# Performance work log

Measured on AMD Instinct MI355X. Metric: run time of the kernel, lower is better.

The kernel has to match this reference:

```python
import jax, jax.numpy as jnp
import numpy as np

NEG_SLOPE = 0.2  # PyG GATConv LeakyReLU slope
HEADS = 4

def _gat_conv(x, edge_index, W, a_src, a_dst, b):
    """Single-relation GATConv (PyG semantics, concat=True).
    x: [N, Fin]; edge_index: [2, E]; W: [Fin, H*D]; a_src/a_dst: [H, D]; b: [H*D].
    """
    N = x.shape[0]
    H, D = a_src.shape
    h = (x @ W).reshape(N, H, D)                      # [N, H, D]
    src, dst = edge_index[0], edge_index[1]
    # per-node attention halves
    al_s = jnp.einsum('nhd,hd->nh', h, a_src)         # [N, H]
    al_d = jnp.einsum('nhd,hd->nh', h, a_dst)         # [N, H]
    alpha = jax.nn.leaky_relu(al_s[src] + al_d[dst], NEG_SLOPE)  # [E, H]
    # segment softmax over incoming edges per destination node
    amax = jax.ops.segment_max(alpha, dst, num_segments=N)       # [N, H]
    e = jnp.exp(alpha - amax[dst])
    denom = jax.ops.segment_sum(e, dst, num_segments=N)          # [N, H]
    w = e / (denom[dst] + 1e-16)                                  # [E, H]
    msg = h[src] * w[:, :, None]                                  # [E, H, D]
    out = jax.ops.segment_sum(msg, dst, num_segments=N)          # [N, H, D]
    return out.reshape(N, H * D) + b

def setup_inputs() -> dict:
    key = jax.random.key(0)
    ks = jax.random.split(key, 8)
    N, Fin, Fout, E, R = 50000, 256, 128, 800000, 3
    return {
        'x': jax.random.normal(ks[0], (N, Fin), dtype=jnp.float32),
        'edge_index_0': jax.random.randint(ks[1], (2, E), 0, N, dtype=jnp.int32),
        'edge_index_1': jax.random.randint(ks[2], (2, E), 0, N, dtype=jnp.int32),
        'edge_index_2': jax.random.randint(ks[3], (2, E), 0, N, dtype=jnp.int32),
        'W': jax.random.normal(ks[4], (R, Fin, Fout), dtype=jnp.float32) * 0.05,
        'att_src': jax.random.normal(ks[5], (R, HEADS, Fout // HEADS), dtype=jnp.float32) * 0.1,
        'att_dst': jax.random.normal(ks[6], (R, HEADS, Fout // HEADS), dtype=jnp.float32) * 0.1,
        'bias': jax.random.normal(ks[7], (R, Fout), dtype=jnp.float32) * 0.01,
    }

def reference(x, edge_index_0, edge_index_1, edge_index_2, W, att_src, att_dst, bias):
    edges = (edge_index_0, edge_index_1, edge_index_2)
    out = None
    for r in range(W.shape[0]):  # small fixed relation loop
        h_rel = _gat_conv(x, edges[r], W[r], att_src[r], att_dst[r], bias[r])
        out = h_rel if out is None else out + h_rel
    return out
```

## Files before the change

kernel.cpp:

```cpp
#include <hip/hip_runtime.h>
#include <hip/hip_bf16.h>

#define NEG_SLOPE 0.2f
#define NBMAX 320
#define KB    512
#define CAP   10240
#define CHUNK 4096

typedef short bf16x8 __attribute__((ext_vector_type(8)));
typedef float f32x4 __attribute__((ext_vector_type(4)));

__device__ inline ushort f2bf(float f) {
  __hip_bfloat16 b = __float2bfloat16(f);
  return *(ushort*)&b;
}
__device__ inline float bf2f(ushort u) {
  unsigned int v = ((unsigned int)u) << 16;
  return *(float*)&v;
}

__global__ __launch_bounds__(256)
void prep_kernel(const float* __restrict__ W,
                 const float* __restrict__ a_src,
                 const float* __restrict__ a_dst,
                 ushort* __restrict__ WbigT) {
  int i = blockIdx.x * 256 + threadIdx.x;
  int c = i >> 8, k = i & 255;
  float v = 0.f;
  if (c < 384) {
    int r = c >> 7, j = c & 127;
    v = W[((size_t)r * 256 + k) * 128 + j];
  } else if (c < 408) {
    int c6 = c - 384, r = c6 >> 3, hh = c6 & 7, hd = hh & 3;
    const float* a = (hh < 4 ? a_src : a_dst) + (r * 4 + hd) * 32;
    const float* wp = W + ((size_t)r * 256 + k) * 128 + hd * 32;
#pragma unroll
    for (int d = 0; d < 32; ++d) v += wp[d] * a[d];
  }
  WbigT[i] = f2bf(v);
}

__global__ __launch_bounds__(256, 2)
void gemm_mfma_kernel(const float* __restrict__ x, const ushort* __restrict__ WT,
                      ushort* __restrict__ hall, float* __restrict__ al, int M) {
  __shared__ __align__(16) ushort As[64][40];
  __shared__ __align__(16) ushort Bs[448][40];
  const int bm = blockIdx.x * 64;
  const int t = threadIdx.x;
  const int l = t & 63;
  const int w = t >> 6;
  const int wm = (w >> 1) * 32;
  const int wn = (w & 1) * 224;
  const int lr = l & 15, lg = l >> 4;

  f32x4 acc[2][14];
#pragma unroll
  for (int i = 0; i < 2; ++i)
#pragma unroll
    for (int j = 0; j < 14; ++j) acc[i][j] = (f32x4){0.f, 0.f, 0.f, 0.f};

  for (int k0 = 0; k0 < 256; k0 += 32) {
    {
      int row = t >> 2, seg = t & 3;
      int grow = bm + row;
      float4 v0 = make_float4(0.f, 0.f, 0.f, 0.f), v1 = v0;
      if (grow < M) {
        const float* xp = x + (size_t)grow * 256 + k0 + seg * 8;
        v0 = *(const float4*)xp;
        v1 = *(const float4*)(xp + 4);
      }
      uint4 pk;
      pk.x = (unsigned)f2bf(v0.x) | ((unsigned)f2bf(v0.y) << 16);
      pk.y = (unsigned)f2bf(v0.z) | ((unsigned)f2bf(v0.w) << 16);
      pk.z = (unsigned)f2bf(v1.x) | ((unsigned)f2bf(v1.y) << 16);
      pk.w = (unsigned)f2bf(v1.z) | ((unsigned)f2bf(v1.w) << 16);
      *(uint4*)&As[row][seg * 8] = pk;
    }
#pragma unroll
    for (int p = 0; p < 7; ++p) {
      int idx = p * 256 + t;
      int nrow = idx >> 2, ch = idx & 3;
      *(uint4*)&Bs[nrow][ch * 8] =
          *(const uint4*)(WT + (size_t)nrow * 256 + k0 + ch * 8);
    }
    __syncthreads();

    bf16x8 afrag[2];
    afrag[0] = *(bf16x8*)&As[wm + lr][lg * 8];
    afrag[1] = *(bf16x8*)&As[wm + 16 + lr][lg * 8];
#pragma unroll
    for (int j = 0; j < 14; ++j) {
      bf16x8 bfrag = *(bf16x8*)&Bs[wn + j * 16 + lr][lg * 8];
      acc[0][j] = __builtin_amdgcn_mfma_f32_16x16x32_bf16(afrag[0], bfrag, acc[0][j], 0, 0, 0);
      acc[1][j] = __builtin_amdgcn_mfma_f32_16x16x32_bf16(afrag[1], bfrag, acc[1][j], 0, 0, 0);
    }
    __syncthreads();
  }

#pragma unroll
  for (int i = 0; i < 2; ++i) {
#pragma unroll
    for (int rr = 0; rr < 4; ++rr) {
      int grow = bm + wm + i * 16 + lg * 4 + rr;
      if (grow >= M) continue;
#pragma unroll
      for (int j = 0; j < 14; ++j) {
        int gcol = wn + j * 16 + lr;
        float c = acc[i][j][rr];
        if (gcol < 384) {
          int rel = gcol >> 7, jj = gcol & 127;
          hall[((size_t)rel * M + grow) * 128 + jj] = f2bf(c);
        } else if (gcol < 408) {
          int c6 = gcol - 384, r = c6 >> 3, hh = c6 & 7;
          al[(((size_t)(hh < 4 ? 0 : 3) + r) * M + grow) * 4 + (hh & 3)] = c;
        }
      }
    }
  }
}

__device__ inline void edge_decode(int i, int E0, int E1,
                                   const int* __restrict__ s0, const int* __restrict__ d0,
                                   const int* __restrict__ s1, const int* __restrict__ d1,
                                   const int* __restrict__ s2, const int* __restrict__ d2,
                                   int N, int& src, int& key) {
  if (i < E0)            { src = s0[i];            key = d0[i]; }
  else if (i < E0 + E1)  { src = s1[i - E0];       key = N + d1[i - E0]; }
  else                   { src = s2[i - E0 - E1];  key = 2 * N + d2[i - E0 - E1]; }
}

__global__ __launch_bounds__(512)
void bucket_stage(const int* __restrict__ s0, const int* __restrict__ d0,
                  const int* __restrict__ s1, const int* __restrict__ d1,
                  const int* __restrict__ s2, const int* __restrict__ d2,
                  int E0, int E1, int E2,
                  int* __restrict__ bcnt, unsigned* __restrict__ staging,
                  int N, int NB) {
  __shared__ ushort es_src[CHUNK];
  __shared__ int    es_key[CHUNK];
  __shared__ int lh[NBMAX], lb[NBMAX];
  const int t = threadIdx.x;
  for (int k = t; k < NB; k += 512) lh[k] = 0;
  __syncthreads();
  const int Etot = E0 + E1 + E2;
  const int lo = blockIdx.x * CHUNK;
  const int hi = min(lo + CHUNK, Etot);
  const int n = hi - lo;
  for (int i = t; i < n; i += 512) {
    int src, key;
    edge_decode(lo + i, E0, E1, s0, d0, s1, d1, s2, d2, N, src, key);
    es_src[i] = (ushort)src;
    es_key[i] = key;
    atomicAdd(&lh[key >> 9], 1);
  }
  __syncthreads();
  for (int k = t; k < NB; k += 512) {
    int v = lh[k];
    lb[k] = v ? (k * CAP + atomicAdd(&bcnt[k], v)) : 0;
    lh[k] = 0;
  }
  __syncthreads();
  for (int i = t; i < n; i += 512) {
    int key = es_key[i];
    int b = key >> 9;
    int pos = lb[b] + atomicAdd(&lh[b], 1);
    if (pos < (b + 1) * CAP)
      staging[pos] = ((unsigned)(key & 511) << 16) | (unsigned)es_src[i];
  }
}

__global__ __launch_bounds__(512)
void bucket_sort(const unsigned* __restrict__ staging, const int* __restrict__ bcnt,
                 int* __restrict__ offs, int* __restrict__ ends,
                 ushort* __restrict__ srt, int n3) {
  __shared__ int cnt[KB];
  __shared__ int cur[KB];
  __shared__ int wsum[8];
  const int b = blockIdx.x;
  const int base = b * KB;
  const int lo = b * CAP;
  const int t = threadIdx.x;
  const int lane = t & 63, wid = t >> 6;
  const int m = min(bcnt[b], CAP);
  cnt[t] = 0;
  __syncthreads();
  for (int i = t; i < m; i += 512)
    atomicAdd(&cnt[staging[lo + i] >> 16], 1);
  __syncthreads();
  int v = cnt[t];
  int sv = v;
#pragma unroll
  for (int d = 1; d < 64; d <<= 1) {
    int u = __shfl_up(sv, d);
    if (lane >= d) sv += u;
  }
  if (lane == 63) wsum[wid] = sv;
  __syncthreads();
  if (t < 8) {
    int ws = wsum[t];
#pragma unroll
    for (int d = 1; d < 8; d <<= 1) {
      int u = __shfl_up(ws, d);
      if (t >= d) ws += u;
    }
    wsum[t] = ws;
  }
  __syncthreads();
  int start = lo + (wid ? wsum[wid - 1] : 0) + sv - v;
  cur[t] = start;
  if (base + t < n3) {
    offs[base + t] = start;
    ends[base + t] = start + v;
  }
  __syncthreads();
  for (int i = t; i < m; i += 512) {
    unsigned p = staging[lo + i];
    int pos = atomicAdd(&cur[p >> 16], 1);
    srt[pos] = (ushort)(p & 0xffffu);
  }
}

__global__ __launch_bounds__(128)
void gat_fused_kernel(const ushort* __restrict__ srt, const int* __restrict__ offs,
                      const int* __restrict__ ends,
                      const ushort* __restrict__ hall,
                      const float* __restrict__ al,
                      const float* __restrict__ bias,
                      float* __restrict__ out, int N) {
  const int d = blockIdx.x;
  const int t = threadIdx.x;
  const int w = t >> 6;
  const int l = t & 63;
  const int eg = l >> 4;
  const int fl = l & 15;
  const int h = fl >> 2;

  __shared__ float slab[3][2][16][9];

#pragma unroll
  for (int rel = 0; rel < 3; ++rel) {
    const int key = rel * N + d;
    const int start = offs[key];
    const int dend = ends[key];
    const float* alS = al + (size_t)rel * N * 4;
    const ushort* hrel = hall + (size_t)rel * N * 128;
    const float ald = al[((size_t)(3 + rel) * N + d) * 4 + h];
    float r0 = 0.f, r1 = 0.f, r2 = 0.f, r3 = 0.f;
    float r4 = 0.f, r5 = 0.f, r6 = 0.f, r7 = 0.f;
    float dl = 0.f;
#pragma unroll 2
    for (int e = start + w * 4 + eg; e < dend; e += 8) {
      int s = srt[e];
      float a = alS[(size_t)s * 4 + h] + ald;
      a = fmaxf(a, NEG_SLOPE * a);
      float ex = __expf(a);
      dl += ex;
      uint4 u = *(const uint4*)(hrel + (size_t)s * 128 + fl * 8);
      r0 += bf2f((ushort)(u.x & 0xffffu)) * ex;
      r1 += bf2f((ushort)(u.x >> 16)) * ex;
      r2 += bf2f((ushort)(u.y & 0xffffu)) * ex;
      r3 += bf2f((ushort)(u.y >> 16)) * ex;
      r4 += bf2f((ushort)(u.z & 0xffffu)) * ex;
      r5 += bf2f((ushort)(u.z >> 16)) * ex;
      r6 += bf2f((ushort)(u.w & 0xffffu)) * ex;
      r7 += bf2f((ushort)(u.w >> 16)) * ex;
    }
    r0 += __shfl_xor(r0, 16); r0 += __shfl_xor(r0, 32);
    r1 += __shfl_xor(r1, 16); r1 += __shfl_xor(r1, 32);
    r2 += __shfl_xor(r2, 16); r2 += __shfl_xor(r2, 32);
    r3 += __shfl_xor(r3, 16); r3 += __shfl_xor(r3, 32);
    r4 += __shfl_xor(r4, 16); r4 += __shfl_xor(r4, 32);
    r5 += __shfl_xor(r5, 16); r5 += __shfl_xor(r5, 32);
    r6 += __shfl_xor(r6, 16); r6 += __shfl_xor(r6, 32);
    r7 += __shfl_xor(r7, 16); r7 += __shfl_xor(r7, 32);
    dl += __shfl_xor(dl, 16); dl += __shfl_xor(dl, 32);
    if (l < 16) {
      slab[rel][w][fl][0] = r0; slab[rel][w][fl][1] = r1;
      slab[rel][w][fl][2] = r2; slab[rel][w][fl][3] = r3;
      slab[rel][w][fl][4] = r4; slab[rel][w][fl][5] = r5;
      slab[rel][w][fl][6] = r6; slab[rel][w][fl][7] = r7;
      slab[rel][w][fl][8] = dl;
    }
  }
  __syncthreads();
  {
    int fl2 = t >> 3, k = t & 7;
    int f = fl2 * 8 + k;
    float o = bias[f] + bias[128 + f] + bias[256 + f];
#pragma unroll
    for (int rel = 0; rel < 3; ++rel) {
      float D = slab[rel][0][fl2][8] + slab[rel][1][fl2][8];
      float R = slab[rel][0][fl2][k] + slab[rel][1][fl2][k];
      o += R / (D + 1e-16f);
    }
    out[(size_t)d * 128 + f] = o;
  }
}

extern "C" void kernel_launch(void* const* d_in, const int* in_sizes, int n_in,
                              void* d_out, int out_size, void* d_ws, size_t ws_size,
                              hipStream_t stream) {
  const float* x     = (const float*)d_in[0];
  const int*   ei[3] = {(const int*)d_in[1], (const int*)d_in[2], (const int*)d_in[3]};
  const float* W     = (const float*)d_in[4];
  const float* a_src = (const float*)d_in[5];
  const float* a_dst = (const float*)d_in[6];
  const float* bias  = (const float*)d_in[7];

  const int Fin = 256;
  const int N = in_sizes[0] / Fin;
  const int E0 = in_sizes[1] / 2, E1 = in_sizes[2] / 2, E2 = in_sizes[3] / 2;
  const int Etot = E0 + E1 + E2;
  const int n3 = 3 * N;
  const int NB = (n3 + KB - 1) / KB;

  float* out = (float*)d_out;

  char* p = (char*)d_ws;
  ushort*   WbigT   = (ushort*)p;    p += (size_t)448 * 256 * 2;
  ushort*   hall    = (ushort*)p;    p += (size_t)N * 384 * 2;
  float*    al      = (float*)p;     p += (size_t)6 * N * 4 * 4;
  unsigned* staging = (unsigned*)p;  p += (size_t)NBMAX * CAP * 4;
  ushort*   srt     = (ushort*)p;    p += (size_t)NBMAX * CAP * 2;
  int*      offs    = (int*)p;       p += (size_t)n3 * 4;
  int*      ends    = (int*)p;       p += (size_t)n3 * 4;
  int*      bcnt    = (int*)p;       p += NBMAX * 4;

  hipMemsetAsync(bcnt, 0, NBMAX * sizeof(int), stream);

  prep_kernel<<<448, 256, 0, stream>>>(W, a_src, a_dst, WbigT);

  gemm_mfma_kernel<<<(N + 63) / 64, 256, 0, stream>>>(x, WbigT, hall, al, N);

  bucket_stage<<<(Etot + CHUNK - 1) / CHUNK, 512, 0, stream>>>(
      ei[0], ei[0] + E0, ei[1], ei[1] + E1, ei[2], ei[2] + E2,
      E0, E1, E2, bcnt, staging, N, NB);

  bucket_sort<<<NB, 512, 0, stream>>>(staging, bcnt, offs, ends, srt, n3);

  gat_fused_kernel<<<N, 128, 0, stream>>>(srt, offs, ends, hall, al, bias, out, N);
}
```

Baseline: 219.4 us.

## Use 32x32x16 MFMA in GEMM, fold bucket-count reset into prep kernel

The GEMM now uses 32x32x16 bf16 MFMA tiles with 7 accumulators per wave instead of 16x16x32 with 28, which cuts LDS fragment reads per MFMA. The hipMemsetAsync of the bucket counters is removed and folded into an extra block of the prep kernel, saving one launch. The bf16-to-float unpack in the gather loop is simplified to a shift or mask per element. The 32x32 output layout scatters its stores differently, and the new epilogue row indexing has to match the MFMA layout exactly for results to stay correct.

```diff
diff --git a/kernel.cpp b/kernel.cpp
--- a/kernel.cpp
+++ b/kernel.cpp
@@ -8,23 +8,27 @@
 #define CHUNK 4096
 
 typedef short bf16x8 __attribute__((ext_vector_type(8)));
-typedef float f32x4 __attribute__((ext_vector_type(4)));
+typedef float f32x4  __attribute__((ext_vector_type(4)));
+typedef float f32x16 __attribute__((ext_vector_type(16)));
 
 __device__ inline ushort f2bf(float f) {
   __hip_bfloat16 b = __float2bfloat16(f);
   return *(ushort*)&b;
-}
-__device__ inline float bf2f(ushort u) {
-  unsigned int v = ((unsigned int)u) << 16;
-  return *(float*)&v;
 }
 
 __global__ __launch_bounds__(256)
 void prep_kernel(const float* __restrict__ W,
                  const float* __restrict__ a_src,
                  const float* __restrict__ a_dst,
-                 ushort* __restrict__ WbigT) {
-  int i = blockIdx.x * 256 + threadIdx.x;
+                 ushort* __restrict__ WbigT,
+                 int* __restrict__ bcnt) {
+  const int b = blockIdx.x;
+  const int t = threadIdx.x;
+  if (b == 448) {
+    for (int k = t; k < NBMAX; k += 256) bcnt[k] = 0;
+    return;
+  }
+  int i = b * 256 + t;
   int c = i >> 8, k = i & 255;
   float v = 0.f;
   if (c < 384) {
@@ -51,13 +55,14 @@
   const int w = t >> 6;
   const int wm = (w >> 1) * 32;
   const int wn = (w & 1) * 224;
-  const int lr = l & 15, lg = l >> 4;
-
-  f32x4 acc[2][14];
-#pragma unroll
-  for (int i = 0; i < 2; ++i)
-#pragma unroll
-    for (int j = 0; j < 14; ++j) acc[i][j] = (f32x4){0.f, 0.f, 0.f, 0.f};
+  const int lr31 = l & 31;
+  const int kg = (l >> 5) * 8;
+
+  f32x16 acc[7];
+#pragma unroll
+  for (int j = 0; j < 7; ++j)
+#pragma unroll
+    for (int r = 0; r < 16; ++r) acc[j][r] = 0.f;
 
   for (int k0 = 0; k0 < 256; k0 += 32) {
     {
@@ -85,35 +90,32 @@
     }
     __syncthreads();
 
-    bf16x8 afrag[2];
-    afrag[0] = *(bf16x8*)&As[wm + lr][lg * 8];
-    afrag[1] = *(bf16x8*)&As[wm + 16 + lr][lg * 8];
-#pragma unroll
-    for (int j = 0; j < 14; ++j) {
-      bf16x8 bfrag = *(bf16x8*)&Bs[wn + j * 16 + lr][lg * 8];
-      acc[0][j] = __builtin_amdgcn_mfma_f32_16x16x32_bf16(afrag[0], bfrag, acc[0][j], 0, 0, 0);
-      acc[1][j] = __builtin_amdgcn_mfma_f32_16x16x32_bf16(afrag[1], bfrag, acc[1][j], 0, 0, 0);
+#pragma unroll
+    for (int kk = 0; kk < 32; kk += 16) {
+      bf16x8 af = *(bf16x8*)&As[wm + lr31][kk + kg];
+#pragma unroll
+      for (int j = 0; j < 7; ++j) {
+        bf16x8 bf = *(bf16x8*)&Bs[wn + j * 32 + lr31][kk + kg];
+        acc[j] = __builtin_amdgcn_mfma_f32_32x32x16_bf16(af, bf, acc[j], 0, 0, 0);
+      }
     }
     __syncthreads();
   }
 
 #pragma unroll
-  for (int i = 0; i < 2; ++i) {
-#pragma unroll
-    for (int rr = 0; rr < 4; ++rr) {
-      int grow = bm + wm + i * 16 + lg * 4 + rr;
+  for (int j = 0; j < 7; ++j) {
+    int gcol = wn + j * 32 + lr31;
+#pragma unroll
+    for (int r = 0; r < 16; ++r) {
+      int grow = bm + wm + (l >> 5) * 4 + (r & 3) + 8 * (r >> 2);
       if (grow >= M) continue;
-#pragma unroll
-      for (int j = 0; j < 14; ++j) {
-        int gcol = wn + j * 16 + lr;
-        float c = acc[i][j][rr];
-        if (gcol < 384) {
-          int rel = gcol >> 7, jj = gcol & 127;
-          hall[((size_t)rel * M + grow) * 128 + jj] = f2bf(c);
-        } else if (gcol < 408) {
-          int c6 = gcol - 384, r = c6 >> 3, hh = c6 & 7;
-          al[(((size_t)(hh < 4 ? 0 : 3) + r) * M + grow) * 4 + (hh & 3)] = c;
-        }
+      float c = acc[j][r];
+      if (gcol < 384) {
+        int rel = gcol >> 7, jj = gcol & 127;
+        hall[((size_t)rel * M + grow) * 128 + jj] = f2bf(c);
+      } else if (gcol < 408) {
+        int c6 = gcol - 384, rr = c6 >> 3, hh = c6 & 7;
+        al[(((size_t)(hh < 4 ? 0 : 3) + rr) * M + grow) * 4 + (hh & 3)] = c;
       }
     }
   }
@@ -256,14 +258,14 @@
       float ex = __expf(a);
       dl += ex;
       uint4 u = *(const uint4*)(hrel + (size_t)s * 128 + fl * 8);
-      r0 += bf2f((ushort)(u.x & 0xffffu)) * ex;
-      r1 += bf2f((ushort)(u.x >> 16)) * ex;
-      r2 += bf2f((ushort)(u.y & 0xffffu)) * ex;
-      r3 += bf2f((ushort)(u.y >> 16)) * ex;
-      r4 += bf2f((ushort)(u.z & 0xffffu)) * ex;
-      r5 += bf2f((ushort)(u.z >> 16)) * ex;
-      r6 += bf2f((ushort)(u.w & 0xffffu)) * ex;
-      r7 += bf2f((ushort)(u.w >> 16)) * ex;
+      r0 += __uint_as_float(u.x << 16) * ex;
+      r1 += __uint_as_float(u.x & 0xffff0000u) * ex;
+      r2 += __uint_as_float(u.y << 16) * ex;
+      r3 += __uint_as_float(u.y & 0xffff0000u) * ex;
+      r4 += __uint_as_float(u.z << 16) * ex;
+      r5 += __uint_as_float(u.z & 0xffff0000u) * ex;
+      r6 += __uint_as_float(u.w << 16) * ex;
+      r7 += __uint_as_float(u.w & 0xffff0000u) * ex;
     }
     r0 += __shfl_xor(r0, 16); r0 += __shfl_xor(r0, 32);
     r1 += __shfl_xor(r1, 16); r1 += __shfl_xor(r1, 32);
@@ -326,9 +328,7 @@
   int*      ends    = (int*)p;       p += (size_t)n3 * 4;
   int*      bcnt    = (int*)p;       p += NBMAX * 4;
 
-  hipMemsetAsync(bcnt, 0, NBMAX * sizeof(int), stream);
-
-  prep_kernel<<<448, 256, 0, stream>>>(W, a_src, a_dst, WbigT);
+  prep_kernel<<<449, 256, 0, stream>>>(W, a_src, a_dst, WbigT, bcnt);
 
   gemm_mfma_kernel<<<(N + 63) / 64, 256, 0, stream>>>(x, WbigT, hall, al, N);
 
```

Result: faster. 212.9 us (-3.0%).
